# Kernel tuning notes

Measured on AMD Instinct MI355X. Metric: run time of the kernel, lower is better.

Reference implementation:

```python
import jax, jax.numpy as jnp
import numpy as np

KS = 3       # kernel_size
STRIDE = 1
PAD = 1

def _conv2d(x, w, b):
    y = jax.lax.conv_general_dilated(
        x, w, window_strides=(STRIDE, STRIDE),
        padding=[(PAD, PAD), (PAD, PAD)],
        dimension_numbers=('NCHW', 'OIHW', 'NCHW'))
    return y + b[None, :, None, None]

def _deform_conv(x, offset, mask, weight):
    # x: (B,C,H,W); offset: (B,2K,Ho,Wo); mask: (B,K,Ho,Wo); weight: (O,C,KS,KS)
    B, C, H, W = x.shape
    K = KS * KS
    Ho, Wo = offset.shape[2], offset.shape[3]
    off = offset.reshape(B, K, 2, Ho, Wo)
    dy, dx = off[:, :, 0], off[:, :, 1]          # (B,K,Ho,Wo)
    ky = jnp.arange(KS).repeat(KS)               # kernel row per tap k
    kx = jnp.tile(jnp.arange(KS), KS)            # kernel col per tap k
    base_y = ky[:, None] + jnp.arange(Ho) * STRIDE - PAD   # (K,Ho)
    base_x = kx[:, None] + jnp.arange(Wo) * STRIDE - PAD   # (K,Wo)
    py = base_y[None, :, :, None].astype(x.dtype) + dy     # (B,K,Ho,Wo)
    px = base_x[None, :, None, :].astype(x.dtype) + dx

    y0 = jnp.floor(py).astype(jnp.int32)
    x0 = jnp.floor(px).astype(jnp.int32)
    wy = py - y0
    wx = px - x0
    x_flat = x.reshape(B, C, H * W)

    def gather(yi, xi):
        valid = (yi >= 0) & (yi < H) & (xi >= 0) & (xi < W)
        yc = jnp.clip(yi, 0, H - 1)
        xc = jnp.clip(xi, 0, W - 1)
        idx = (yc * W + xc).reshape(B, 1, -1)
        v = jnp.take_along_axis(x_flat, idx, axis=2).reshape(B, C, K, Ho, Wo)
        return v * valid[:, None].astype(x.dtype)

    w00 = ((1 - wy) * (1 - wx))[:, None]
    w01 = ((1 - wy) * wx)[:, None]
    w10 = (wy * (1 - wx))[:, None]
    w11 = (wy * wx)[:, None]
    val = (gather(y0, x0) * w00 + gather(y0, x0 + 1) * w01 +
           gather(y0 + 1, x0) * w10 + gather(y0 + 1, x0 + 1) * w11)
    val = val * mask[:, None]                    # modulated samples (B,C,K,Ho,Wo)
    O = weight.shape[0]
    return jnp.einsum('bckhw,ock->bohw', val, weight.reshape(O, C, K))

def setup_inputs() -> dict:
    key = jax.random.key(0)
    ks = jax.random.split(key, 6)
    B, C, H, W, O = 8, 64, 128, 128, 64
    x = jax.random.normal(ks[0], (B, C, H, W), dtype=jnp.float32)
    # small scales so offsets/modulators are in a realistic (trained-ish) range
    offset_w = 0.05 * jax.random.normal(ks[1], (2 * KS * KS, C, KS, KS), dtype=jnp.float32)
    offset_b = 0.05 * jax.random.normal(ks[2], (2 * KS * KS,), dtype=jnp.float32)
    mod_w = 0.05 * jax.random.normal(ks[3], (KS * KS, C, KS, KS), dtype=jnp.float32)
    mod_b = 0.05 * jax.random.normal(ks[4], (KS * KS,), dtype=jnp.float32)
    weight = (1.0 / np.sqrt(C * KS * KS)) * jax.random.normal(ks[5], (O, C, KS, KS), dtype=jnp.float32)
    return {"x": x, "offset_w": offset_w, "offset_b": offset_b,
            "mod_w": mod_w, "mod_b": mod_b, "weight": weight}

def reference(x, offset_w, offset_b, mod_w, mod_b, weight):
    h, w = x.shape[2], x.shape[3]
    max_offset = max(h, w) / 4.0
    offset = jnp.clip(_conv2d(x, offset_w, offset_b), -max_offset, max_offset)
    modulator = 2.0 * jax.nn.sigmoid(_conv2d(x, mod_w, mod_b))
    return _deform_conv(x, offset, modulator, weight)
```

## Files before the change

### kernel.cpp

```cpp
#include <hip/hip_runtime.h>
#include <math.h>

#define B_ 8
#define C_ 64
#define H_ 128
#define W_ 128
#define O_ 64
#define HW (H_*W_)

typedef float f32x4 __attribute__((ext_vector_type(4)));
typedef float f32x2 __attribute__((ext_vector_type(2)));
typedef short s16x8 __attribute__((ext_vector_type(8)));

#define XT_BUF   0
#define WBFA_BUF 4194304
#define WBFB_BUF 4203520

__device__ __forceinline__ unsigned short f2bf(float f) {
    union { float f; unsigned u; } v; v.f = f;
    unsigned r = (v.u + 0x7FFFu + ((v.u >> 16) & 1u)) >> 16;
    return (unsigned short)r;
}
__device__ __forceinline__ unsigned cvt_pk_bf16(float lo, float hi) {
    unsigned r;
    asm("v_cvt_pk_bf16_f32 %0, %1, %2" : "=v"(r) : "v"(lo), "v"(hi));
    return r;
}
__device__ __forceinline__ f32x2 bfpair(s16x8 v, int i) {
    union { s16x8 s; unsigned u[4]; } c; c.s = v;
    unsigned r = c.u[i];
    union { unsigned u; float f; } lo, hi;
    lo.u = r << 16;
    hi.u = r & 0xFFFF0000u;
    f32x2 out; out.x = lo.f; out.y = hi.f;
    return out;
}
__device__ __forceinline__ void gload_lds16(const void* g, void* l) {
    __builtin_amdgcn_global_load_lds(
        (const __attribute__((address_space(1))) unsigned int*)g,
        (__attribute__((address_space(3))) unsigned int*)l, 16, 0, 0);
}

__global__ void prep_weights(const float* __restrict__ offw,
                             const float* __restrict__ modw,
                             const float* __restrict__ w,
                             float* __restrict__ ws) {
    int t = blockIdx.x * 256 + threadIdx.x;
    unsigned short* wbfA = (unsigned short*)(ws + WBFA_BUF);
    unsigned short* wbfB = (unsigned short*)(ws + WBFB_BUF);
    if (t < 18432) {
        int j = t & 7, lane = (t >> 3) & 63, nt = (t >> 9) & 1, ks = (t >> 10) & 1, tap = t >> 11;
        int c = ks * 32 + ((lane >> 4) & 3) * 8 + j;
        int oc = nt * 16 + (lane & 15);
        float v = 0.f;
        if (oc < 18)      v = offw[oc * (C_ * 9) + c * 9 + tap];
        else if (oc < 27) v = modw[(oc - 18) * (C_ * 9) + c * 9 + tap];
        wbfA[t] = f2bf(v);
    } else {
        int t2 = t - 18432;
        if (t2 < 36864) {
            int j = t2 & 7, lane = (t2 >> 3) & 63, nt = (t2 >> 9) & 3, ks = (t2 >> 11) & 1, tap = t2 >> 12;
            int c = ks * 32 + ((lane >> 4) & 3) * 8 + j;
            int o = nt * 16 + (lane & 15);
            wbfB[t2] = f2bf(w[o * (C_ * 9) + c * 9 + tap]);
        }
    }
}

__global__ __launch_bounds__(256) void transpose_x(const float* __restrict__ x,
                                                   float* __restrict__ ws) {
    __shared__ float lds[64 * 65];
    int b = blockIdx.x & 7;
    int chunk = (blockIdx.y << 5) | (blockIdx.x >> 3);
    int p0 = chunk * 64;
    int t = threadIdx.x;
    int pl = t & 63;
    const float* xb = x + (size_t)b * C_ * HW + p0;
#pragma unroll
    for (int i = 0; i < 16; i++) {
        int c = (t >> 6) + i * 4;
        lds[c * 65 + pl] = __builtin_nontemporal_load(&xb[(size_t)c * HW + pl]);
    }
    __syncthreads();
    unsigned short* xo = (unsigned short*)(ws + XT_BUF) + ((size_t)b * HW + p0) * 64;
#pragma unroll
    for (int pass = 0; pass < 2; pass++) {
        int p = (t >> 3) + pass * 32;
        int c0 = (t & 7) * 8;
        union { unsigned short u[8]; s16x8 v; } pk;
#pragma unroll
        for (int j = 0; j < 8; j++) pk.u[j] = f2bf(lds[(c0 + j) * 65 + p]);
        *(s16x8*)(xo + (size_t)p * 64 + c0) = pk.v;
    }
}

__global__ __launch_bounds__(1024) void fused(const float* __restrict__ ws,
                                              const float* __restrict__ offb,
                                              const float* __restrict__ modb,
                                              float* __restrict__ out) {
    __shared__ s16x8 xtile_v[5832];
    __shared__ float offL[16][18][16];
    __shared__ float mskL[16][9][16];
    __shared__ char wlds[36864];
    char* xtile = (char*)xtile_v;
    int t = threadIdx.x;
    int wv = t >> 6, l = t & 63;
    int b = blockIdx.x & 7;
    int tile = (blockIdx.y << 3) | (blockIdx.x >> 3);
    int ty = tile >> 3, tx = tile & 7;
    int t0y = ty * 16, t0x = tx * 16;
    int y = t0y + wv, x0 = t0x;
    int pw = y * W_ + x0;
    int pl = l & 15, csub = l >> 4;

    const unsigned short* xtb = (const unsigned short*)(ws + XT_BUF) + (size_t)b * HW * 64;
    const s16x8* wbfA = (const s16x8*)(ws + WBFA_BUF);
    const s16x8* wbfB = (const s16x8*)(ws + WBFB_BUF);
    const char* wsrcB = (const char*)(ws + WBFB_BUF);

#pragma unroll
    for (int i = 0; i < 3; i++) {
        int ch = wv + i * 16;
        if (ch < 36) {
            int tk = ch >> 1, ntl = ch & 1;
            gload_lds16(wsrcB + (size_t)(tk * 4 + ntl) * 1024 + l * 16, wlds + ch * 1024);
        }
    }
#pragma unroll
    for (int k = 0; k < 6; k++) {
        int i = t + k * 1024;
        if (i < 5832) {
            int p = i >> 3, w8 = i & 7;
            int r = p / 27, cc = p - r * 27;
            int gr = min(max(t0y - 5 + r, 0), H_ - 1);
            int gc = min(max(t0x - 5 + cc, 0), W_ - 1);
            s16x8 v = *(const s16x8*)(xtb + (size_t)((gr << 7) + gc) * 64 + (w8 << 3));
            *(s16x8*)(xtile + p * 128 + ((w8 ^ (p & 7)) << 4)) = v;
        }
    }
    __syncthreads();

    {
        int oc0 = pl, oc1 = 16 + pl;
        float bi0 = offb[oc0];
        float bi1 = (oc1 < 18) ? offb[oc1] : (oc1 < 27 ? modb[oc1 - 18] : 0.f);
        f32x4 acc0 = {bi0, bi0, bi0, bi0};
        f32x4 acc1 = {bi1, bi1, bi1, bi1};
        const s16x8 zf = {0, 0, 0, 0, 0, 0, 0, 0};

        for (int tap = 0; tap < 9; tap++) {
            int ys = y + tap / 3 - 1;
            int xs = x0 + pl + tap % 3 - 1;
            bool vld = ((unsigned)ys < (unsigned)H_) && ((unsigned)xs < (unsigned)W_);
            int yc = min(max(ys, 0), H_ - 1);
            int xc = min(max(xs, 0), W_ - 1);
            int sp = (yc - t0y + 5) * 27 + (xc - t0x + 5);
            s16x8 a0 = *(const s16x8*)(xtile + sp * 128 + ((csub ^ (sp & 7)) << 4));
            s16x8 a1 = *(const s16x8*)(xtile + sp * 128 + (((4 + csub) ^ (sp & 7)) << 4));
            a0 = vld ? a0 : zf;
            a1 = vld ? a1 : zf;
            s16x8 b00 = wbfA[((tap * 2 + 0) * 2 + 0) * 64 + l];
            s16x8 b01 = wbfA[((tap * 2 + 0) * 2 + 1) * 64 + l];
            s16x8 b10 = wbfA[((tap * 2 + 1) * 2 + 0) * 64 + l];
            s16x8 b11 = wbfA[((tap * 2 + 1) * 2 + 1) * 64 + l];
            acc0 = __builtin_amdgcn_mfma_f32_16x16x32_bf16(a0, b00, acc0, 0, 0, 0);
            acc1 = __builtin_amdgcn_mfma_f32_16x16x32_bf16(a0, b01, acc1, 0, 0, 0);
            acc0 = __builtin_amdgcn_mfma_f32_16x16x32_bf16(a1, b10, acc0, 0, 0, 0);
            acc1 = __builtin_amdgcn_mfma_f32_16x16x32_bf16(a1, b11, acc1, 0, 0, 0);
        }

#pragma unroll
        for (int j = 0; j < 4; j++)
            offL[wv][oc0][csub * 4 + j] = fminf(fmaxf(acc0[j], -32.f), 32.f);
        if (oc1 < 18) {
#pragma unroll
            for (int j = 0; j < 4; j++)
                offL[wv][oc1][csub * 4 + j] = fminf(fmaxf(acc1[j], -32.f), 32.f);
        } else if (oc1 < 27) {
#pragma unroll
            for (int j = 0; j < 4; j++)
                mskL[wv][oc1 - 18][csub * 4 + j] = 2.f / (1.f + __expf(-acc1[j]));
        }
    }
    __syncthreads();

    int xx = x0 + pl;
    const unsigned short* xtb2 = xtb + csub * 8;

    float dyv[9], dxv[9], mmv[9];
#pragma unroll
    for (int tap = 0; tap < 9; tap++) {
        dyv[tap] = offL[wv][2 * tap][pl];
        dxv[tap] = offL[wv][2 * tap + 1][pl];
        mmv[tap] = mskL[wv][tap][pl];
    }

    f32x4 acc[4];
#pragma unroll
    for (int nt = 0; nt < 4; nt++) acc[nt] = (f32x4)0.f;

#pragma unroll
    for (int tap = 0; tap < 9; tap++) {
        float py = (float)(y + tap / 3 - 1) + dyv[tap];
        float px = (float)(xx + tap % 3 - 1) + dxv[tap];
        float mm = mmv[tap];
        float fy = floorf(py), fx = floorf(px);
        int y0 = (int)fy, xq = (int)fx;
        float wy = py - fy, wx = px - fx;
        bool vy0 = (unsigned)y0 < (unsigned)H_;
        bool vy1 = (unsigned)(y0 + 1) < (unsigned)H_;
        bool vx0 = (unsigned)xq < (unsigned)W_;
        bool vx1 = (unsigned)(xq + 1) < (unsigned)W_;
        int yc0 = min(max(y0, 0), H_ - 1), yc1 = min(max(y0 + 1, 0), H_ - 1);
        int xc0 = min(max(xq, 0), W_ - 1), xc1 = min(max(xq + 1, 0), W_ - 1);
        float e0 = (1.f - wy) * (1.f - wx) * mm * ((vy0 && vx0) ? 1.f : 0.f);
        float e1 = (1.f - wy) * wx         * mm * ((vy0 && vx1) ? 1.f : 0.f);
        float e2 = wy * (1.f - wx)         * mm * ((vy1 && vx0) ? 1.f : 0.f);
        float e3 = wy * wx                 * mm * ((vy1 && vx1) ? 1.f : 0.f);

        int sy0 = yc0 - t0y + 5, sy1 = yc1 - t0y + 5;
        int sx0 = xc0 - t0x + 5, sx1 = xc1 - t0x + 5;
        bool inb = ((unsigned)sy0 < 27u) && ((unsigned)sy1 < 27u) &&
                   ((unsigned)sx0 < 27u) && ((unsigned)sx1 < 27u);
        int cy0 = min(max(sy0, 0), 26), cy1 = min(max(sy1, 0), 26);
        int cx0 = min(max(sx0, 0), 26), cx1 = min(max(sx1, 0), 26);
        int q00 = cy0 * 27 + cx0, q01 = cy0 * 27 + cx1;
        int q10 = cy1 * 27 + cx0, q11 = cy1 * 27 + cx1;

        s16x8 g00a = *(const s16x8*)(xtile + q00 * 128 + ((csub ^ (q00 & 7)) << 4));
        s16x8 g00b = *(const s16x8*)(xtile + q00 * 128 + (((4 + csub) ^ (q00 & 7)) << 4));
        s16x8 g01a = *(const s16x8*)(xtile + q01 * 128 + ((csub ^ (q01 & 7)) << 4));
        s16x8 g01b = *(const s16x8*)(xtile + q01 * 128 + (((4 + csub) ^ (q01 & 7)) << 4));
        s16x8 g10a = *(const s16x8*)(xtile + q10 * 128 + ((csub ^ (q10 & 7)) << 4));
        s16x8 g10b = *(const s16x8*)(xtile + q10 * 128 + (((4 + csub) ^ (q10 & 7)) << 4));
        s16x8 g11a = *(const s16x8*)(xtile + q11 * 128 + ((csub ^ (q11 & 7)) << 4));
        s16x8 g11b = *(const s16x8*)(xtile + q11 * 128 + (((4 + csub) ^ (q11 & 7)) << 4));

        if (!inb) {
            const unsigned short* p00 = xtb2 + (size_t)(yc0 * W_ + xc0) * 64;
            const unsigned short* p01 = xtb2 + (size_t)(yc0 * W_ + xc1) * 64;
            const unsigned short* p10 = xtb2 + (size_t)(yc1 * W_ + xc0) * 64;
            const unsigned short* p11 = xtb2 + (size_t)(yc1 * W_ + xc1) * 64;
            g00a = *(const s16x8*)p00; g00b = *(const s16x8*)(p00 + 32);
            g01a = *(const s16x8*)p01; g01b = *(const s16x8*)(p01 + 32);
            g10a = *(const s16x8*)p10; g10b = *(const s16x8*)(p10 + 32);
            g11a = *(const s16x8*)p11; g11b = *(const s16x8*)(p11 + 32);
        }

        f32x2 e0v = {e0, e0}, e1v = {e1, e1}, e2v = {e2, e2}, e3v = {e3, e3};
        union { unsigned u[4]; s16x8 v; } A0, A1;
#pragma unroll
        for (int q = 0; q < 4; q++) {
            f32x2 va = e0v * bfpair(g00a, q) + e1v * bfpair(g01a, q)
                     + e2v * bfpair(g10a, q) + e3v * bfpair(g11a, q);
            A0.u[q] = cvt_pk_bf16(va.x, va.y);
            f32x2 vb = e0v * bfpair(g00b, q) + e1v * bfpair(g01b, q)
                     + e2v * bfpair(g10b, q) + e3v * bfpair(g11b, q);
            A1.u[q] = cvt_pk_bf16(vb.x, vb.y);
        }
#pragma unroll
        for (int nt = 0; nt < 4; nt++) {
            s16x8 bf0, bf1;
            if (nt < 2) {
                bf0 = *(const s16x8*)(wlds + ((tap * 2 + 0) * 2 + nt) * 1024 + l * 16);
                bf1 = *(const s16x8*)(wlds + ((tap * 2 + 1) * 2 + nt) * 1024 + l * 16);
            } else {
                bf0 = wbfB[((tap * 2 + 0) * 4 + nt) * 64 + l];
                bf1 = wbfB[((tap * 2 + 1) * 4 + nt) * 64 + l];
            }
            acc[nt] = __builtin_amdgcn_mfma_f32_16x16x32_bf16(A0.v, bf0, acc[nt], 0, 0, 0);
            acc[nt] = __builtin_amdgcn_mfma_f32_16x16x32_bf16(A1.v, bf1, acc[nt], 0, 0, 0);
        }
    }

    float* ob = out + (size_t)b * O_ * HW;
    int gp0 = pw + csub * 4;
#pragma unroll
    for (int nt = 0; nt < 4; nt++) {
        int oc = nt * 16 + pl;
        *(f32x4*)(ob + (size_t)oc * HW + gp0) = acc[nt];
    }
}

extern "C" void kernel_launch(void* const* d_in, const int* in_sizes, int n_in,
                              void* d_out, int out_size, void* d_ws, size_t ws_size,
                              hipStream_t stream) {
    const float* x    = (const float*)d_in[0];
    const float* offw = (const float*)d_in[1];
    const float* offb = (const float*)d_in[2];
    const float* modw = (const float*)d_in[3];
    const float* modb = (const float*)d_in[4];
    const float* w    = (const float*)d_in[5];
    float* out = (float*)d_out;
    float* ws  = (float*)d_ws;

    prep_weights<<<dim3(216), dim3(256), 0, stream>>>(offw, modw, w, ws);
    transpose_x<<<dim3(HW / 64, B_), dim3(256), 0, stream>>>(x, ws);
    fused<<<dim3(64, 8), dim3(1024), 0, stream>>>(ws, offb, modb, out);
}
```

Before: 69.02 us.

## Shrink input halo and stage all deform-conv weights in LDS

Reduces the LDS input tile halo from 5 to 3 pixels (22x22 instead of 27x27), which cuts halo loading per block. The freed LDS holds all 72 weight chunks, so the main MFMA loop reads every B fragment from LDS instead of fetching half of them from global memory. It also drops the barrier between the offset/mask writes and their reads, since each wave reads only its own rows. The cost is that sampled offsets beyond the smaller halo fall back to slower global gathers, and total LDS use now sits very close to the per-CU limit.

```diff
diff --git a/kernel.cpp b/kernel.cpp
--- a/kernel.cpp
+++ b/kernel.cpp
@@ -7,6 +7,10 @@
 #define W_ 128
 #define O_ 64
 #define HW (H_*W_)
+
+#define HALO 3
+#define TDIM 22
+#define TPX  (TDIM*TDIM)
 
 typedef float f32x4 __attribute__((ext_vector_type(4)));
 typedef float f32x2 __attribute__((ext_vector_type(2)));
@@ -98,10 +102,10 @@
                                               const float* __restrict__ offb,
                                               const float* __restrict__ modb,
                                               float* __restrict__ out) {
-    __shared__ s16x8 xtile_v[5832];
+    __shared__ s16x8 xtile_v[TPX * 8];
     __shared__ float offL[16][18][16];
     __shared__ float mskL[16][9][16];
-    __shared__ char wlds[36864];
+    __shared__ char wlds[73728];
     char* xtile = (char*)xtile_v;
     int t = threadIdx.x;
     int wv = t >> 6, l = t & 63;
@@ -115,25 +119,22 @@
 
     const unsigned short* xtb = (const unsigned short*)(ws + XT_BUF) + (size_t)b * HW * 64;
     const s16x8* wbfA = (const s16x8*)(ws + WBFA_BUF);
-    const s16x8* wbfB = (const s16x8*)(ws + WBFB_BUF);
     const char* wsrcB = (const char*)(ws + WBFB_BUF);
 
 #pragma unroll
-    for (int i = 0; i < 3; i++) {
+    for (int i = 0; i < 5; i++) {
         int ch = wv + i * 16;
-        if (ch < 36) {
-            int tk = ch >> 1, ntl = ch & 1;
-            gload_lds16(wsrcB + (size_t)(tk * 4 + ntl) * 1024 + l * 16, wlds + ch * 1024);
-        }
-    }
-#pragma unroll
-    for (int k = 0; k < 6; k++) {
+        if (ch < 72)
+            gload_lds16(wsrcB + (size_t)ch * 1024 + l * 16, wlds + ch * 1024);
+    }
+#pragma unroll
+    for (int k = 0; k < 4; k++) {
         int i = t + k * 1024;
-        if (i < 5832) {
+        if (i < TPX * 8) {
             int p = i >> 3, w8 = i & 7;
-            int r = p / 27, cc = p - r * 27;
-            int gr = min(max(t0y - 5 + r, 0), H_ - 1);
-            int gc = min(max(t0x - 5 + cc, 0), W_ - 1);
+            int r = p / TDIM, cc = p - r * TDIM;
+            int gr = min(max(t0y - HALO + r, 0), H_ - 1);
+            int gc = min(max(t0x - HALO + cc, 0), W_ - 1);
             s16x8 v = *(const s16x8*)(xtb + (size_t)((gr << 7) + gc) * 64 + (w8 << 3));
             *(s16x8*)(xtile + p * 128 + ((w8 ^ (p & 7)) << 4)) = v;
         }
@@ -154,7 +155,7 @@
             bool vld = ((unsigned)ys < (unsigned)H_) && ((unsigned)xs < (unsigned)W_);
             int yc = min(max(ys, 0), H_ - 1);
             int xc = min(max(xs, 0), W_ - 1);
-            int sp = (yc - t0y + 5) * 27 + (xc - t0x + 5);
+            int sp = (yc - t0y + HALO) * TDIM + (xc - t0x + HALO);
             s16x8 a0 = *(const s16x8*)(xtile + sp * 128 + ((csub ^ (sp & 7)) << 4));
             s16x8 a1 = *(const s16x8*)(xtile + sp * 128 + (((4 + csub) ^ (sp & 7)) << 4));
             a0 = vld ? a0 : zf;
@@ -182,7 +183,6 @@
                 mskL[wv][oc1 - 18][csub * 4 + j] = 2.f / (1.f + __expf(-acc1[j]));
         }
     }
-    __syncthreads();
 
     int xx = x0 + pl;
     const unsigned short* xtb2 = xtb + csub * 8;
@@ -218,14 +218,14 @@
         float e2 = wy * (1.f - wx)         * mm * ((vy1 && vx0) ? 1.f : 0.f);
         float e3 = wy * wx                 * mm * ((vy1 && vx1) ? 1.f : 0.f);
 
-        int sy0 = yc0 - t0y + 5, sy1 = yc1 - t0y + 5;
-        int sx0 = xc0 - t0x + 5, sx1 = xc1 - t0x + 5;
-        bool inb = ((unsigned)sy0 < 27u) && ((unsigned)sy1 < 27u) &&
-                   ((unsigned)sx0 < 27u) && ((unsigned)sx1 < 27u);
-        int cy0 = min(max(sy0, 0), 26), cy1 = min(max(sy1, 0), 26);
-        int cx0 = min(max(sx0, 0), 26), cx1 = min(max(sx1, 0), 26);
-        int q00 = cy0 * 27 + cx0, q01 = cy0 * 27 + cx1;
-        int q10 = cy1 * 27 + cx0, q11 = cy1 * 27 + cx1;
+        int sy0 = yc0 - t0y + HALO, sy1 = yc1 - t0y + HALO;
+        int sx0 = xc0 - t0x + HALO, sx1 = xc1 - t0x + HALO;
+        bool inb = ((unsigned)sy0 < (unsigned)TDIM) && ((unsigned)sy1 < (unsigned)TDIM) &&
+                   ((unsigned)sx0 < (unsigned)TDIM) && ((unsigned)sx1 < (unsigned)TDIM);
+        int cy0 = min(max(sy0, 0), TDIM - 1), cy1 = min(max(sy1, 0), TDIM - 1);
+        int cx0 = min(max(sx0, 0), TDIM - 1), cx1 = min(max(sx1, 0), TDIM - 1);
+        int q00 = cy0 * TDIM + cx0, q01 = cy0 * TDIM + cx1;
+        int q10 = cy1 * TDIM + cx0, q11 = cy1 * TDIM + cx1;
 
         s16x8 g00a = *(const s16x8*)(xtile + q00 * 128 + ((csub ^ (q00 & 7)) << 4));
         s16x8 g00b = *(const s16x8*)(xtile + q00 * 128 + (((4 + csub) ^ (q00 & 7)) << 4));
@@ -260,14 +260,8 @@
         }
 #pragma unroll
         for (int nt = 0; nt < 4; nt++) {
-            s16x8 bf0, bf1;
-            if (nt < 2) {
-                bf0 = *(const s16x8*)(wlds + ((tap * 2 + 0) * 2 + nt) * 1024 + l * 16);
-                bf1 = *(const s16x8*)(wlds + ((tap * 2 + 1) * 2 + nt) * 1024 + l * 16);
-            } else {
-                bf0 = wbfB[((tap * 2 + 0) * 4 + nt) * 64 + l];
-                bf1 = wbfB[((tap * 2 + 1) * 4 + nt) * 64 + l];
-            }
+            s16x8 bf0 = *(const s16x8*)(wlds + ((tap * 2 + 0) * 4 + nt) * 1024 + l * 16);
+            s16x8 bf1 = *(const s16x8*)(wlds + ((tap * 2 + 1) * 4 + nt) * 1024 + l * 16);
             acc[nt] = __builtin_amdgcn_mfma_f32_16x16x32_bf16(A0.v, bf0, acc[nt], 0, 0, 0);
             acc[nt] = __builtin_amdgcn_mfma_f32_16x16x32_bf16(A1.v, bf1, acc[nt], 0, 0, 0);
         }
```

New measurement: 64.37 us. 1.07x faster.
